# Kernel tuning notes

Hardware: AMD Instinct MI355X
Metric: run time of the kernel (lower is better)

## Reference

```python
import jax, jax.numpy as jnp
import numpy as np

B, T, D, K = 16, 4096, 128, 1024
BETA = 0.25


def setup_inputs() -> dict:
    key = jax.random.key(0)
    k1, k2 = jax.random.split(key)
    z_e = jax.random.normal(k1, (B, T, D), dtype=jnp.float32)
    # tf.random.uniform default: U[0, 1)
    vecs_embedding = jax.random.uniform(k2, (K, D), dtype=jnp.float32)
    return {"z_e": z_e, "vecs_embedding": vecs_embedding}


def reference(z_e, vecs_embedding):
    # dot_z_embedding: [B, T, K]
    dot = jnp.einsum('btd,kd->btk', z_e, vecs_embedding)
    norm_sq_z = jnp.sum(jnp.square(z_e), axis=-1)              # [B, T]
    norm_sq_e = jnp.sum(jnp.square(vecs_embedding), axis=-1)   # [K]
    dist = -2.0 * dot + norm_sq_z[..., None] + norm_sq_e       # [B, T, K]
    ids = jnp.argmin(dist, axis=-1)                            # [B, T]
    z_q = vecs_embedding[ids]                                  # [B, T, D]
    # tf.norm over channel axis (axes[0] == 2), then mean over batch*time
    loss_commit = jnp.mean(jnp.linalg.norm(jax.lax.stop_gradient(z_e) - z_q, axis=-1))
    loss_codebook = jnp.mean(jnp.linalg.norm(z_e - jax.lax.stop_gradient(z_q), axis=-1))
    loss = loss_codebook + BETA * loss_commit
    similarity = dot / jnp.sqrt(norm_sq_z)[..., None] / jnp.sqrt(norm_sq_e)
    return z_q, similarity, ids, loss
```

## Files before the change

### kernel.cpp

```cpp
#include <hip/hip_runtime.h>
#include <math.h>

#define MTOT 65536
#define DD   128
#define KK   1024
#define BETA 0.25f
#define TM   64
#define NCH  64

typedef __attribute__((ext_vector_type(8))) short short8;
typedef __attribute__((ext_vector_type(4))) float float4v;

__device__ __forceinline__ unsigned bf16_rne(float x) {
    unsigned u = __float_as_uint(x);
    return (u + 0x7fffu + ((u >> 16) & 1u)) >> 16;
}

__device__ __forceinline__ void gload_lds16(const void* g, void* l) {
    __builtin_amdgcn_global_load_lds(
        (const __attribute__((address_space(1))) unsigned int*)g,
        (__attribute__((address_space(3))) unsigned int*)l, 16, 0, 0);
}

__global__ void k_norms(const float* __restrict__ e, ushort* __restrict__ bp,
                        float* __restrict__ nef, float* __restrict__ inef,
                        float* __restrict__ loss) {
    const int gw = blockIdx.x * 4 + (threadIdx.x >> 6);
    const int lane = threadIdx.x & 63;
    char* hb = (char*)bp;
    char* lb = hb + 262144;
    const int sub = lane & 3;
    for (int code = gw; code < KK; code += 256) {
        float2 ev = ((const float2*)(e + (size_t)code * DD))[lane];
        unsigned h0 = bf16_rne(ev.x), h1 = bf16_rne(ev.y);
        float l0f = ev.x - __uint_as_float(h0 << 16);
        float l1f = ev.y - __uint_as_float(h1 << 16);
        ushort2 hv; hv.x = (ushort)h0; hv.y = (ushort)h1;
        ushort2 lv; lv.x = (ushort)bf16_rne(l0f); lv.y = (ushort)bf16_rne(l1f);
        int sw = (((lane >> 2) * 16) ^ ((code & 7) << 4)) + sub * 4;
        *(ushort2*)(hb + code * 256 + sw) = hv;
        *(ushort2*)(lb + code * 256 + sw) = lv;
        float s = ev.x * ev.x + ev.y * ev.y;
        #pragma unroll
        for (int off = 32; off; off >>= 1) s += __shfl_down(s, off, 64);
        if (lane == 0) { nef[code] = s; inef[code] = 1.0f / sqrtf(s); }
    }
    if (blockIdx.x == 0 && threadIdx.x == 0) *loss = 0.0f;
}

__launch_bounds__(256, 2)
__global__ void k_main(const float* __restrict__ z, float* __restrict__ sim,
                       const ushort* __restrict__ bpre,
                       const float* __restrict__ nef, const float* __restrict__ inef,
                       const float* __restrict__ e, float* __restrict__ zq,
                       float* __restrict__ idsf, float* __restrict__ loss) {
    __shared__ __align__(16) ushort Bs[2 * 16384];
    __shared__ float nzv[TM], inzv[TM];
    __shared__ unsigned candL[TM];
    __shared__ float bs[4];

    const int t = threadIdx.x;
    const int w = t >> 6, lane = t & 63, cl = lane & 15, q = lane >> 4;
    const int mh = (w & 1) * 32, nh = (w >> 1) * 32;
    const int r0 = blockIdx.x * TM;

    auto STAGE = [&](int buf, int ch2) {
        const char* gb = (const char*)bpre + (size_t)ch2 * 16384;
        #pragma unroll
        for (int i = 0; i < 8; ++i) {
            int slot = i * 256 + t;
            int goff = slot * 16 + ((slot >= 1024) ? 245760 : 0);
            gload_lds16(gb + goff,
                        (char*)Bs + buf * 32768 + (i * 256 + (t & 0xFFC0)) * 16);
        }
    };

    STAGE(0, 0);

    short8 afh[2][4], afl[2][4];
    float pn0 = 0.0f, pn1 = 0.0f;
    const char* zb = (const char*)z;
    #pragma unroll
    for (int mt = 0; mt < 2; ++mt) {
        const char* rp = zb + (size_t)(r0 + mh + mt * 16 + cl) * 512;
        #pragma unroll
        for (int s = 0; s < 4; ++s) {
            float4v f0 = *(const float4v*)(rp + s * 128 + q * 32);
            float4v f1 = *(const float4v*)(rp + s * 128 + q * 32 + 16);
            short8 h, l;
            float ps = 0.0f;
            #pragma unroll
            for (int j = 0; j < 4; ++j) {
                float fx = f0[j];
                unsigned hu = bf16_rne(fx);
                h[j] = (short)hu;
                l[j] = (short)bf16_rne(fx - __uint_as_float(hu << 16));
                ps += fx * fx;
                float fy = f1[j];
                unsigned hw2 = bf16_rne(fy);
                h[j + 4] = (short)hw2;
                l[j + 4] = (short)bf16_rne(fy - __uint_as_float(hw2 << 16));
                ps += fy * fy;
            }
            afh[mt][s] = h; afl[mt][s] = l;
            if (mt == 0) pn0 += ps; else pn1 += ps;
        }
    }
    pn0 += __shfl_xor(pn0, 16, 64); pn0 += __shfl_xor(pn0, 32, 64);
    pn1 += __shfl_xor(pn1, 16, 64); pn1 += __shfl_xor(pn1, 32, 64);
    if (q == 0) {
        nzv[mh + cl]      = pn0; inzv[mh + cl]      = 1.0f / sqrtf(pn0);
        nzv[mh + 16 + cl] = pn1; inzv[mh + 16 + cl] = 1.0f / sqrtf(pn1);
    }
    __syncthreads();

    float nzr[8], inzr[8];
    #pragma unroll
    for (int mt = 0; mt < 2; ++mt)
        #pragma unroll
        for (int r = 0; r < 4; ++r) {
            int rl = mh + mt * 16 + q * 4 + r;
            nzr[mt * 4 + r] = nzv[rl]; inzr[mt * 4 + r] = inzv[rl];
        }

    float b1v[8], b2v[8]; int b1i[8], b2i[8];
    #pragma unroll
    for (int s = 0; s < 8; ++s) { b1v[s] = 3.4e38f; b2v[s] = 3.4e38f; b1i[s] = 0; b2i[s] = 0; }

    const int swz = (cl & 7) << 4;
    for (int ch = 0; ch < 16; ++ch) {
        const int c0 = ch * NCH;
        const char* Bb = (const char*)Bs + (ch & 1) * 32768;
        if (ch < 15) STAGE((ch + 1) & 1, ch + 1);

        float nec[2], inec[2];
        #pragma unroll
        for (int nt = 0; nt < 2; ++nt) {
            int c = c0 + nh + nt * 16 + cl;
            nec[nt] = nef[c]; inec[nt] = inef[c];
        }

        float4v acc[2][2];
        #pragma unroll
        for (int mt = 0; mt < 2; ++mt)
            #pragma unroll
            for (int nt = 0; nt < 2; ++nt) acc[mt][nt] = (float4v)(0.0f);

        short8 bh0[4], bh1[4];
        #pragma unroll
        for (int s = 0; s < 4; ++s) {
            const int ko = (s * 64 + q * 16) ^ swz;
            bh0[s] = *(const short8*)(Bb + (nh + cl) * 256 + ko);
            bh1[s] = *(const short8*)(Bb + (nh + 16 + cl) * 256 + ko);
            acc[0][0] = __builtin_amdgcn_mfma_f32_16x16x32_bf16(afh[0][s], bh0[s], acc[0][0], 0, 0, 0);
            acc[0][1] = __builtin_amdgcn_mfma_f32_16x16x32_bf16(afh[0][s], bh1[s], acc[0][1], 0, 0, 0);
            acc[1][0] = __builtin_amdgcn_mfma_f32_16x16x32_bf16(afh[1][s], bh0[s], acc[1][0], 0, 0, 0);
            acc[1][1] = __builtin_amdgcn_mfma_f32_16x16x32_bf16(afh[1][s], bh1[s], acc[1][1], 0, 0, 0);
        }
        #pragma unroll
        for (int s = 0; s < 4; ++s) {
            const int ko = (s * 64 + q * 16) ^ swz;
            short8 bl0 = *(const short8*)(Bb + 16384 + (nh + cl) * 256 + ko);
            short8 bl1 = *(const short8*)(Bb + 16384 + (nh + 16 + cl) * 256 + ko);
            acc[0][0] = __builtin_amdgcn_mfma_f32_16x16x32_bf16(afh[0][s], bl0, acc[0][0], 0, 0, 0);
            acc[0][1] = __builtin_amdgcn_mfma_f32_16x16x32_bf16(afh[0][s], bl1, acc[0][1], 0, 0, 0);
            acc[1][0] = __builtin_amdgcn_mfma_f32_16x16x32_bf16(afh[1][s], bl0, acc[1][0], 0, 0, 0);
            acc[1][1] = __builtin_amdgcn_mfma_f32_16x16x32_bf16(afh[1][s], bl1, acc[1][1], 0, 0, 0);
        }
        #pragma unroll
        for (int s = 0; s < 4; ++s) {
            acc[0][0] = __builtin_amdgcn_mfma_f32_16x16x32_bf16(afl[0][s], bh0[s], acc[0][0], 0, 0, 0);
            acc[0][1] = __builtin_amdgcn_mfma_f32_16x16x32_bf16(afl[0][s], bh1[s], acc[0][1], 0, 0, 0);
            acc[1][0] = __builtin_amdgcn_mfma_f32_16x16x32_bf16(afl[1][s], bh0[s], acc[1][0], 0, 0, 0);
            acc[1][1] = __builtin_amdgcn_mfma_f32_16x16x32_bf16(afl[1][s], bh1[s], acc[1][1], 0, 0, 0);
        }

        __syncthreads();

        #pragma unroll
        for (int mt = 0; mt < 2; ++mt)
            #pragma unroll
            for (int r = 0; r < 4; ++r) {
                const int slot = mt * 4 + r;
                const size_t rowg = (size_t)(r0 + mh + mt * 16 + q * 4 + r);
                #pragma unroll
                for (int nt = 0; nt < 2; ++nt) {
                    float dot = acc[mt][nt][r];
                    int col = c0 + nh + nt * 16 + cl;
                    sim[rowg * KK + col] = dot * inzr[slot] * inec[nt];
                    float dist = fmaf(-2.0f, dot, nzr[slot] + nec[nt]);
                    if (dist < b1v[slot]) {
                        b2v[slot] = b1v[slot]; b2i[slot] = b1i[slot];
                        b1v[slot] = dist;      b1i[slot] = col;
                    } else if (dist < b2v[slot]) {
                        b2v[slot] = dist; b2i[slot] = col;
                    }
                }
            }
    }

    float* redv = (float*)Bs;
    int*   redi = (int*)(Bs + 16384);
    #pragma unroll
    for (int mt = 0; mt < 2; ++mt)
        #pragma unroll
        for (int r = 0; r < 4; ++r) {
            int slot = mt * 4 + r;
            int rl = mh + mt * 16 + q * 4 + r;
            int ei = rl * 64 + ((w >> 1) * 16 + cl) * 2;
            redv[ei] = b1v[slot]; redv[ei + 1] = b2v[slot];
            redi[ei] = b1i[slot]; redi[ei + 1] = b2i[slot];
        }
    __syncthreads();
    if (t < TM) {
        float B1v = 3.4e38f, B2v = 3.4e38f; int B1i = 0x7fffffff, B2i = 0x7fffffff;
        for (int j = 0; j < 64; ++j) {
            float v = redv[t * 64 + j]; int ii = redi[t * 64 + j];
            if (v < B1v || (v == B1v && ii < B1i)) { B2v = B1v; B2i = B1i; B1v = v; B1i = ii; }
            else if (v < B2v || (v == B2v && ii < B2i)) { B2v = v; B2i = ii; }
        }
        candL[t] = (unsigned)B1i | ((unsigned)B2i << 16);
    }
    __syncthreads();

    float wsum = 0.0f;
    const int rloc = w * 16;
    for (int i = 0; i < 16; ++i) {
        int row = r0 + rloc + i;
        unsigned pk = candL[rloc + i];
        int c1 = (int)(pk & 0xffffu), c2 = (int)(pk >> 16);
        float2 zv = ((const float2*)(z + (size_t)row * DD))[lane];
        float2 e1 = ((const float2*)(e + (size_t)c1 * DD))[lane];
        float2 e2 = ((const float2*)(e + (size_t)c2 * DD))[lane];
        float v0 = zv.x * zv.x + zv.y * zv.y;
        float v1 = zv.x * e1.x + zv.y * e1.y;
        float v2 = zv.x * e2.x + zv.y * e2.y;
        float v3 = e1.x * e1.x + e1.y * e1.y;
        float v4 = e2.x * e2.x + e2.y * e2.y;
        #pragma unroll
        for (int off = 32; off; off >>= 1) {
            v0 += __shfl_down(v0, off, 64);
            v1 += __shfl_down(v1, off, 64);
            v2 += __shfl_down(v2, off, 64);
            v3 += __shfl_down(v3, off, 64);
            v4 += __shfl_down(v4, off, 64);
        }
        int choice = 0; float ssq = 0.0f;
        if (lane == 0) {
            float d1 = fmaf(-2.0f, v1, v0 + v3);
            float d2 = fmaf(-2.0f, v2, v0 + v4);
            choice = (d2 < d1 || (d2 == d1 && c2 < c1)) ? 1 : 0;
            ssq = choice ? d2 : d1;
        }
        choice = __shfl(choice, 0, 64);
        float2 es; es.x = choice ? e2.x : e1.x; es.y = choice ? e2.y : e1.y;
        int cs = choice ? c2 : c1;
        ((float2*)(zq + (size_t)row * DD))[lane] = es;
        if (lane == 0) {
            wsum += sqrtf(fmaxf(ssq, 0.0f));
            idsf[row] = (float)cs;
        }
    }
    if (lane == 0) bs[w] = wsum;
    __syncthreads();
    if (t == 0)
        atomicAdd(loss, (bs[0] + bs[1] + bs[2] + bs[3]) * ((1.0f + BETA) / (float)MTOT));
}

extern "C" void kernel_launch(void* const* d_in, const int* in_sizes, int n_in,
                              void* d_out, int out_size, void* d_ws, size_t ws_size,
                              hipStream_t stream) {
    const float* z = (const float*)d_in[0];
    const float* e = (const float*)d_in[1];
    float* out  = (float*)d_out;
    float* zq   = out;
    float* sim  = out + (size_t)MTOT * DD;
    float* idsf = sim + (size_t)MTOT * KK;
    float* loss = idsf + MTOT;

    ushort* bpre = (ushort*)d_ws;
    float*  nef  = (float*)((char*)d_ws + 524288);
    float*  inef = nef + 1024;

    k_norms<<<64,        256, 0, stream>>>(e, bpre, nef, inef, loss);
    k_main <<<MTOT / TM, 256, 0, stream>>>(z, sim, bpre, nef, inef, e, zq, idsf, loss);
}
```

Before: 455.7 us.

## Swap MFMA operands so lanes own rows; vectorize sim stores, shuffle argmin reduce

The MFMA operand order is swapped so each lane's accumulator holds four consecutive codebook columns for a single z row. This lets the similarity output be written as 16-byte float4 stores instead of scalar stores, and cuts the per-lane top-2 tracking from 8 rows to 2. The row norm is dropped from the distance because it is constant per row and does not affect the argmin. The cross-lane top-2 merge now uses wave shuffles plus a small LDS merge instead of a 64-entry serial scan, at the cost of some tie-breaking subtlety in the merged candidate order.

```diff
diff --git a/kernel.cpp b/kernel.cpp
--- a/kernel.cpp
+++ b/kernel.cpp
@@ -48,6 +48,19 @@
     if (blockIdx.x == 0 && threadIdx.x == 0) *loss = 0.0f;
 }
 
+__device__ __forceinline__ void merge2(float& v1, int& i1, float& v2, int& i2,
+                                       float ov1, int oi1, float ov2, int oi2) {
+    bool l1 = (ov1 < v1) || (ov1 == v1 && oi1 < i1);
+    if (l1) {
+        bool l2 = (ov2 < v1) || (ov2 == v1 && oi2 < i1);
+        v2 = l2 ? ov2 : v1; i2 = l2 ? oi2 : i1;
+        v1 = ov1; i1 = oi1;
+    } else {
+        bool l2 = (ov1 < v2) || (ov1 == v2 && oi1 < i2);
+        if (l2) { v2 = ov1; i2 = oi1; }
+    }
+}
+
 __launch_bounds__(256, 2)
 __global__ void k_main(const float* __restrict__ z, float* __restrict__ sim,
                        const ushort* __restrict__ bpre,
@@ -55,7 +68,6 @@
                        const float* __restrict__ e, float* __restrict__ zq,
                        float* __restrict__ idsf, float* __restrict__ loss) {
     __shared__ __align__(16) ushort Bs[2 * 16384];
-    __shared__ float nzv[TM], inzv[TM];
     __shared__ unsigned candL[TM];
     __shared__ float bs[4];
 
@@ -108,24 +120,12 @@
     }
     pn0 += __shfl_xor(pn0, 16, 64); pn0 += __shfl_xor(pn0, 32, 64);
     pn1 += __shfl_xor(pn1, 16, 64); pn1 += __shfl_xor(pn1, 32, 64);
-    if (q == 0) {
-        nzv[mh + cl]      = pn0; inzv[mh + cl]      = 1.0f / sqrtf(pn0);
-        nzv[mh + 16 + cl] = pn1; inzv[mh + 16 + cl] = 1.0f / sqrtf(pn1);
-    }
+    float inzr[2]; inzr[0] = 1.0f / sqrtf(pn0); inzr[1] = 1.0f / sqrtf(pn1);
     __syncthreads();
 
-    float nzr[8], inzr[8];
+    float b1v[2], b2v[2]; int b1i[2], b2i[2];
     #pragma unroll
-    for (int mt = 0; mt < 2; ++mt)
-        #pragma unroll
-        for (int r = 0; r < 4; ++r) {
-            int rl = mh + mt * 16 + q * 4 + r;
-            nzr[mt * 4 + r] = nzv[rl]; inzr[mt * 4 + r] = inzv[rl];
-        }
-
-    float b1v[8], b2v[8]; int b1i[8], b2i[8];
-    #pragma unroll
-    for (int s = 0; s < 8; ++s) { b1v[s] = 3.4e38f; b2v[s] = 3.4e38f; b1i[s] = 0; b2i[s] = 0; }
+    for (int s = 0; s < 2; ++s) { b1v[s] = 3.4e38f; b2v[s] = 3.4e38f; b1i[s] = 0; b2i[s] = 0; }
 
     const int swz = (cl & 7) << 4;
     for (int ch = 0; ch < 16; ++ch) {
@@ -133,18 +133,19 @@
         const char* Bb = (const char*)Bs + (ch & 1) * 32768;
         if (ch < 15) STAGE((ch + 1) & 1, ch + 1);
 
-        float nec[2], inec[2];
-        #pragma unroll
-        for (int nt = 0; nt < 2; ++nt) {
-            int c = c0 + nh + nt * 16 + cl;
-            nec[nt] = nef[c]; inec[nt] = inef[c];
+        float4v ne4[2], ine4[2];
+        #pragma unroll
+        for (int ct = 0; ct < 2; ++ct) {
+            int cb = c0 + nh + ct * 16 + q * 4;
+            ne4[ct]  = *(const float4v*)(nef + cb);
+            ine4[ct] = *(const float4v*)(inef + cb);
         }
 
         float4v acc[2][2];
         #pragma unroll
-        for (int mt = 0; mt < 2; ++mt)
+        for (int ct = 0; ct < 2; ++ct)
             #pragma unroll
-            for (int nt = 0; nt < 2; ++nt) acc[mt][nt] = (float4v)(0.0f);
+            for (int zt = 0; zt < 2; ++zt) acc[ct][zt] = (float4v)(0.0f);
 
         short8 bh0[4], bh1[4];
         #pragma unroll
@@ -152,74 +153,88 @@
             const int ko = (s * 64 + q * 16) ^ swz;
             bh0[s] = *(const short8*)(Bb + (nh + cl) * 256 + ko);
             bh1[s] = *(const short8*)(Bb + (nh + 16 + cl) * 256 + ko);
-            acc[0][0] = __builtin_amdgcn_mfma_f32_16x16x32_bf16(afh[0][s], bh0[s], acc[0][0], 0, 0, 0);
-            acc[0][1] = __builtin_amdgcn_mfma_f32_16x16x32_bf16(afh[0][s], bh1[s], acc[0][1], 0, 0, 0);
-            acc[1][0] = __builtin_amdgcn_mfma_f32_16x16x32_bf16(afh[1][s], bh0[s], acc[1][0], 0, 0, 0);
-            acc[1][1] = __builtin_amdgcn_mfma_f32_16x16x32_bf16(afh[1][s], bh1[s], acc[1][1], 0, 0, 0);
+            acc[0][0] = __builtin_amdgcn_mfma_f32_16x16x32_bf16(bh0[s], afh[0][s], acc[0][0], 0, 0, 0);
+            acc[0][1] = __builtin_amdgcn_mfma_f32_16x16x32_bf16(bh0[s], afh[1][s], acc[0][1], 0, 0, 0);
+            acc[1][0] = __builtin_amdgcn_mfma_f32_16x16x32_bf16(bh1[s], afh[0][s], acc[1][0], 0, 0, 0);
+            acc[1][1] = __builtin_amdgcn_mfma_f32_16x16x32_bf16(bh1[s], afh[1][s], acc[1][1], 0, 0, 0);
         }
         #pragma unroll
         for (int s = 0; s < 4; ++s) {
             const int ko = (s * 64 + q * 16) ^ swz;
             short8 bl0 = *(const short8*)(Bb + 16384 + (nh + cl) * 256 + ko);
             short8 bl1 = *(const short8*)(Bb + 16384 + (nh + 16 + cl) * 256 + ko);
-            acc[0][0] = __builtin_amdgcn_mfma_f32_16x16x32_bf16(afh[0][s], bl0, acc[0][0], 0, 0, 0);
-            acc[0][1] = __builtin_amdgcn_mfma_f32_16x16x32_bf16(afh[0][s], bl1, acc[0][1], 0, 0, 0);
-            acc[1][0] = __builtin_amdgcn_mfma_f32_16x16x32_bf16(afh[1][s], bl0, acc[1][0], 0, 0, 0);
-            acc[1][1] = __builtin_amdgcn_mfma_f32_16x16x32_bf16(afh[1][s], bl1, acc[1][1], 0, 0, 0);
+            acc[0][0] = __builtin_amdgcn_mfma_f32_16x16x32_bf16(bl0, afh[0][s], acc[0][0], 0, 0, 0);
+            acc[0][1] = __builtin_amdgcn_mfma_f32_16x16x32_bf16(bl0, afh[1][s], acc[0][1], 0, 0, 0);
+            acc[1][0] = __builtin_amdgcn_mfma_f32_16x16x32_bf16(bl1, afh[0][s], acc[1][0], 0, 0, 0);
+            acc[1][1] = __builtin_amdgcn_mfma_f32_16x16x32_bf16(bl1, afh[1][s], acc[1][1], 0, 0, 0);
         }
         #pragma unroll
         for (int s = 0; s < 4; ++s) {
-            acc[0][0] = __builtin_amdgcn_mfma_f32_16x16x32_bf16(afl[0][s], bh0[s], acc[0][0], 0, 0, 0);
-            acc[0][1] = __builtin_amdgcn_mfma_f32_16x16x32_bf16(afl[0][s], bh1[s], acc[0][1], 0, 0, 0);
-            acc[1][0] = __builtin_amdgcn_mfma_f32_16x16x32_bf16(afl[1][s], bh0[s], acc[1][0], 0, 0, 0);
-            acc[1][1] = __builtin_amdgcn_mfma_f32_16x16x32_bf16(afl[1][s], bh1[s], acc[1][1], 0, 0, 0);
+            acc[0][0] = __builtin_amdgcn_mfma_f32_16x16x32_bf16(bh0[s], afl[0][s], acc[0][0], 0, 0, 0);
+            acc[0][1] = __builtin_amdgcn_mfma_f32_16x16x32_bf16(bh0[s], afl[1][s], acc[0][1], 0, 0, 0);
+            acc[1][0] = __builtin_amdgcn_mfma_f32_16x16x32_bf16(bh1[s], afl[0][s], acc[1][0], 0, 0, 0);
+            acc[1][1] = __builtin_amdgcn_mfma_f32_16x16x32_bf16(bh1[s], afl[1][s], acc[1][1], 0, 0, 0);
         }
 
         __syncthreads();
 
         #pragma unroll
-        for (int mt = 0; mt < 2; ++mt)
+        for (int zt = 0; zt < 2; ++zt) {
+            const float inz = inzr[zt];
+            const size_t rowg = (size_t)(r0 + mh + zt * 16 + cl);
             #pragma unroll
-            for (int r = 0; r < 4; ++r) {
-                const int slot = mt * 4 + r;
-                const size_t rowg = (size_t)(r0 + mh + mt * 16 + q * 4 + r);
+            for (int ct = 0; ct < 2; ++ct) {
+                const int cb = c0 + nh + ct * 16 + q * 4;
+                float4v d = acc[ct][zt];
+                float4v sv;
                 #pragma unroll
-                for (int nt = 0; nt < 2; ++nt) {
-                    float dot = acc[mt][nt][r];
-                    int col = c0 + nh + nt * 16 + cl;
-                    sim[rowg * KK + col] = dot * inzr[slot] * inec[nt];
-                    float dist = fmaf(-2.0f, dot, nzr[slot] + nec[nt]);
-                    if (dist < b1v[slot]) {
-                        b2v[slot] = b1v[slot]; b2i[slot] = b1i[slot];
-                        b1v[slot] = dist;      b1i[slot] = col;
-                    } else if (dist < b2v[slot]) {
-                        b2v[slot] = dist; b2i[slot] = col;
+                for (int j = 0; j < 4; ++j) sv[j] = d[j] * inz * ine4[ct][j];
+                *(float4v*)(sim + rowg * KK + cb) = sv;
+                #pragma unroll
+                for (int j = 0; j < 4; ++j) {
+                    float dist = fmaf(-2.0f, d[j], ne4[ct][j]);
+                    int col = cb + j;
+                    if (dist < b1v[zt]) {
+                        b2v[zt] = b1v[zt]; b2i[zt] = b1i[zt];
+                        b1v[zt] = dist;    b1i[zt] = col;
+                    } else if (dist < b2v[zt]) {
+                        b2v[zt] = dist; b2i[zt] = col;
                     }
                 }
             }
-    }
-
-    float* redv = (float*)Bs;
-    int*   redi = (int*)(Bs + 16384);
+        }
+    }
+
     #pragma unroll
-    for (int mt = 0; mt < 2; ++mt)
-        #pragma unroll
-        for (int r = 0; r < 4; ++r) {
-            int slot = mt * 4 + r;
-            int rl = mh + mt * 16 + q * 4 + r;
-            int ei = rl * 64 + ((w >> 1) * 16 + cl) * 2;
-            redv[ei] = b1v[slot]; redv[ei + 1] = b2v[slot];
-            redi[ei] = b1i[slot]; redi[ei + 1] = b2i[slot];
-        }
+    for (int zt = 0; zt < 2; ++zt) {
+        #pragma unroll
+        for (int off = 16; off <= 32; off <<= 1) {
+            float ov1 = __shfl_xor(b1v[zt], off, 64);
+            int   oi1 = __shfl_xor(b1i[zt], off, 64);
+            float ov2 = __shfl_xor(b2v[zt], off, 64);
+            int   oi2 = __shfl_xor(b2i[zt], off, 64);
+            merge2(b1v[zt], b1i[zt], b2v[zt], b2i[zt], ov1, oi1, ov2, oi2);
+        }
+    }
+    float* top = (float*)Bs;
+    if (q == 0) {
+        #pragma unroll
+        for (int zt = 0; zt < 2; ++zt) {
+            int row = mh + zt * 16 + cl;
+            float4v v;
+            v[0] = b1v[zt]; v[1] = __int_as_float(b1i[zt]);
+            v[2] = b2v[zt]; v[3] = __int_as_float(b2i[zt]);
+            *(float4v*)(top + (row * 2 + (w >> 1)) * 4) = v;
+        }
+    }
     __syncthreads();
     if (t < TM) {
-        float B1v = 3.4e38f, B2v = 3.4e38f; int B1i = 0x7fffffff, B2i = 0x7fffffff;
-        for (int j = 0; j < 64; ++j) {
-            float v = redv[t * 64 + j]; int ii = redi[t * 64 + j];
-            if (v < B1v || (v == B1v && ii < B1i)) { B2v = B1v; B2i = B1i; B1v = v; B1i = ii; }
-            else if (v < B2v || (v == B2v && ii < B2i)) { B2v = v; B2i = ii; }
-        }
-        candL[t] = (unsigned)B1i | ((unsigned)B2i << 16);
+        float4v e0 = *(const float4v*)(top + (t * 2 + 0) * 4);
+        float4v e1 = *(const float4v*)(top + (t * 2 + 1) * 4);
+        float v1 = e0[0], v2 = e0[2];
+        int   i1 = __float_as_int(e0[1]), i2 = __float_as_int(e0[3]);
+        merge2(v1, i1, v2, i2, e1[0], __float_as_int(e1[1]), e1[2], __float_as_int(e1[3]));
+        candL[t] = (unsigned)i1 | ((unsigned)i2 << 16);
     }
     __syncthreads();
 
```

Measured after the change: 491.2 us. +7.8%, slower.
